# Kernel tuning notes

Hardware: AMD Instinct MI355X
Metric: run time of the kernel (lower is better)

Reference implementation:

```python
import jax, jax.numpy as jnp
import numpy as np

WS = 10      # window_size
HID = 32     # hidden_dim
B, T = 1024, 4096


def setup_inputs() -> dict:
    key = jax.random.key(0)
    k = jax.random.split(key, 7)
    returns = jax.random.normal(k[0], (B, T), dtype=jnp.float32) * 0.01
    W1 = jax.random.normal(k[1], (WS, HID), dtype=jnp.float32) * (1.0 / np.sqrt(WS))
    b1 = jnp.zeros((HID,), dtype=jnp.float32)
    W2 = jax.random.normal(k[2], (HID, HID), dtype=jnp.float32) * (1.0 / np.sqrt(HID))
    b2 = jnp.zeros((HID,), dtype=jnp.float32)
    W3 = jax.random.normal(k[3], (HID, 1), dtype=jnp.float32) * (1.0 / np.sqrt(HID))
    b3 = jnp.zeros((1,), dtype=jnp.float32)
    return {"returns": returns, "W1": W1, "b1": b1, "W2": W2, "b2": b2, "W3": W3, "b3": b3}


def reference(returns, W1, b1, W2, b2, W3, b3):
    ws = W1.shape[0]
    Bb, Tt = returns.shape
    # Unfold all sliding windows at once: windows[b, i, :] = returns[b, i:i+ws]
    # (window ending just before timestep t = i + ws)
    idx = jnp.arange(Tt - ws)[:, None] + jnp.arange(ws)[None, :]  # [T-ws, ws]
    windows = returns[:, idx]                                     # [B, T-ws, ws]
    h = jax.nn.relu(windows @ W1 + b1)                            # [B, T-ws, HID]
    h = jax.nn.relu(h @ W2 + b2)                                  # [B, T-ws, HID]
    out = 0.5 * jax.nn.sigmoid((h @ W3 + b3).squeeze(-1))         # [B, T-ws]
    # H_local[:, t] = out[:, t-ws] for t >= ws; first ws columns copy column ws
    head = jnp.broadcast_to(out[:, :1], (Bb, ws))                 # [B, ws]
    return jnp.concatenate([head, out], axis=1)                   # [B, T]
```

## Files before the change

kernel.cpp:

```cpp
#include <hip/hip_runtime.h>
#include <math.h>

typedef _Float16 f16x8  __attribute__((ext_vector_type(8)));
typedef _Float16 h2v    __attribute__((ext_vector_type(2)));
typedef float    f32x16 __attribute__((ext_vector_type(16)));
typedef float    f32x4  __attribute__((ext_vector_type(4)));
typedef __fp16   h2a    __attribute__((ext_vector_type(2)));
typedef unsigned u32x4  __attribute__((ext_vector_type(4)));

#define WS    10
#define HID   32
#define BDIM  256
#define NWAVE 4
#define GN    32
#define T_LEN 4096
#define NGRP  (T_LEN / GN)

__device__ inline unsigned pack2u(float a, float b) {
    h2a t = __builtin_amdgcn_cvt_pkrtz(a, b);
    return __builtin_bit_cast(unsigned, t);
}
__device__ inline unsigned relu2(unsigned u) {
    h2v x = __builtin_bit_cast(h2v, u);
    h2v z = {(_Float16)0.0f, (_Float16)0.0f};
    return __builtin_bit_cast(unsigned, __builtin_elementwise_max(x, z));
}

__global__ __launch_bounds__(BDIM, 4)
void hurst_row5(const float* __restrict__ returns,
                const float* __restrict__ W1, const float* __restrict__ b1,
                const float* __restrict__ W2, const float* __restrict__ b2,
                const float* __restrict__ W3, const float* __restrict__ b3,
                float* __restrict__ out)
{
    const int tid  = threadIdx.x;
    const int wid  = tid >> 6;
    const int lane = tid & 63;
    const int n    = lane & 31;
    const int hi   = lane >> 5;

    f32x16 b1v, b2v, b3v;
    #pragma unroll
    for (int i = 0; i < 4; ++i) {
        const f32x4 v1 = ((const f32x4*)b1)[2 * i + hi];
        const f32x4 v2 = ((const f32x4*)b2)[2 * i + hi];
        #pragma unroll
        for (int o = 0; o < 4; ++o) {
            b1v[4 * i + o] = v1[o];
            b2v[4 * i + o] = v2[o];
        }
    }
    const float b3s = b3[0];
    #pragma unroll
    for (int r = 0; r < 16; ++r) b3v[r] = b3s;

    f16x8 a1, a2lo, a2hi, a3lo, a3hi;
    #pragma unroll
    for (int jj = 0; jj < 8; ++jj) {
        const int k  = 8 * hi + jj;
        a1[jj] = (k < WS) ? (_Float16)W1[k * HID + n] : (_Float16)0.0f;
        const int kf = (k & 3) | ((k & 4) << 1) | ((k & 8) >> 1);
        a2lo[jj] = (_Float16)W2[kf * HID + n];
        a2hi[jj] = (_Float16)W2[(16 + kf) * HID + n];
        a3lo[jj] = (_Float16)W3[kf];
        a3hi[jj] = (_Float16)W3[16 + kf];
    }

    const float* rptr = returns + (size_t)blockIdx.x * T_LEN;
    float*       optr = out     + (size_t)blockIdx.x * T_LEN;

    const int t0  = wid * GN + n;
    int ws_c = (t0 >= WS) ? (t0 - WS) : 0;
    float e2_c[2], v6_c[6];
    __builtin_memcpy(e2_c, &rptr[ws_c + 8 * hi], 8);
    __builtin_memcpy(v6_c, &rptr[ws_c + 2], 24);

    for (int g = wid; g < NGRP; g += NWAVE) {
        const int gn_ = (g + NWAVE < NGRP) ? (g + NWAVE) : g;
        const int tn  = gn_ * GN + n;
        const int wsn = (tn >= WS) ? (tn - WS) : 0;
        float e2_n[2], v6_n[6];
        __builtin_memcpy(e2_n, &rptr[wsn + 8 * hi], 8);
        __builtin_memcpy(v6_n, &rptr[wsn + 2], 24);

        u32x4 xu;
        xu[0] = pack2u(e2_c[0], e2_c[1]);
        xu[1] = hi ? 0u : pack2u(v6_c[0], v6_c[1]);
        xu[2] = hi ? 0u : pack2u(v6_c[2], v6_c[3]);
        xu[3] = hi ? 0u : pack2u(v6_c[4], v6_c[5]);
        const f16x8 xb = __builtin_bit_cast(f16x8, xu);

        f32x16 d1 = __builtin_amdgcn_mfma_f32_32x32x16_f16(a1, xb, b1v, 0, 0, 0);

        u32x4 p1lo, p1hi;
        #pragma unroll
        for (int i = 0; i < 4; ++i) {
            p1lo[i] = relu2(pack2u(d1[2 * i],     d1[2 * i + 1]));
            p1hi[i] = relu2(pack2u(d1[8 + 2 * i], d1[9 + 2 * i]));
        }

        f32x16 d2 = __builtin_amdgcn_mfma_f32_32x32x16_f16(
                        a2lo, __builtin_bit_cast(f16x8, p1lo), b2v, 0, 0, 0);
        d2 = __builtin_amdgcn_mfma_f32_32x32x16_f16(
                        a2hi, __builtin_bit_cast(f16x8, p1hi), d2, 0, 0, 0);

        u32x4 p2lo, p2hi;
        #pragma unroll
        for (int i = 0; i < 4; ++i) {
            p2lo[i] = relu2(pack2u(d2[2 * i],     d2[2 * i + 1]));
            p2hi[i] = relu2(pack2u(d2[8 + 2 * i], d2[9 + 2 * i]));
        }

        f32x16 d3 = __builtin_amdgcn_mfma_f32_32x32x16_f16(
                        a3lo, __builtin_bit_cast(f16x8, p2lo), b3v, 0, 0, 0);
        d3 = __builtin_amdgcn_mfma_f32_32x32x16_f16(
                        a3hi, __builtin_bit_cast(f16x8, p2hi), d3, 0, 0, 0);

        const float o = 0.5f * __builtin_amdgcn_rcpf(1.0f + __expf(-d3[0]));
        if (hi == 0)
            optr[g * GN + n] = o;

        #pragma unroll
        for (int i = 0; i < 2; ++i) e2_c[i] = e2_n[i];
        #pragma unroll
        for (int i = 0; i < 6; ++i) v6_c[i] = v6_n[i];
    }
}

extern "C" void kernel_launch(void* const* d_in, const int* in_sizes, int n_in,
                              void* d_out, int out_size, void* d_ws, size_t ws_size,
                              hipStream_t stream) {
    const float* returns = (const float*)d_in[0];
    const float* W1      = (const float*)d_in[1];
    const float* b1      = (const float*)d_in[2];
    const float* W2      = (const float*)d_in[3];
    const float* b2      = (const float*)d_in[4];
    const float* W3      = (const float*)d_in[5];
    const float* b3      = (const float*)d_in[6];
    float* out = (float*)d_out;

    const int B = out_size / T_LEN;

    dim3 grid(B, 1, 1);
    dim3 block(BDIM, 1, 1);
    hurst_row5<<<grid, block, 0, stream>>>(returns, W1, b1, W2, b2, W3, b3, out);
}
```

Measured before the change: 101.8 us.

## Switch to grid-stride work distribution over all groups with persistent grid

Replaces the one-block-per-row mapping with a fixed grid of 1280 blocks whose waves stride over all 32-timestep groups across every row. Occupancy hint rises to 5 blocks per CU, the software prefetch of the next window is dropped, and the window loads are restructured into two 16-byte loads. The b3 bias vector register is removed by reusing b2v as the d3 accumulator and subtracting a scalar correction. The batch size of 1024 is hardcoded, so the kernel ignores out_size, and the prefetch removal exposes load latency.

```diff
diff --git a/kernel.cpp b/kernel.cpp
--- a/kernel.cpp
+++ b/kernel.cpp
@@ -8,13 +8,16 @@
 typedef __fp16   h2a    __attribute__((ext_vector_type(2)));
 typedef unsigned u32x4  __attribute__((ext_vector_type(4)));
 
-#define WS    10
-#define HID   32
-#define BDIM  256
-#define NWAVE 4
-#define GN    32
-#define T_LEN 4096
-#define NGRP  (T_LEN / GN)
+#define WS     10
+#define HID    32
+#define BDIM   256
+#define NWAVE  4
+#define GN     32
+#define T_LEN  4096
+#define GPR    (T_LEN / GN)
+#define NGTOT  (GPR * 1024)
+#define GRID   1280
+#define WSTRIDE (GRID * NWAVE)
 
 __device__ inline unsigned pack2u(float a, float b) {
     h2a t = __builtin_amdgcn_cvt_pkrtz(a, b);
@@ -26,12 +29,12 @@
     return __builtin_bit_cast(unsigned, __builtin_elementwise_max(x, z));
 }
 
-__global__ __launch_bounds__(BDIM, 4)
-void hurst_row5(const float* __restrict__ returns,
-                const float* __restrict__ W1, const float* __restrict__ b1,
-                const float* __restrict__ W2, const float* __restrict__ b2,
-                const float* __restrict__ W3, const float* __restrict__ b3,
-                float* __restrict__ out)
+__global__ __launch_bounds__(BDIM, 5)
+void hurst_wave5(const float* __restrict__ returns,
+                 const float* __restrict__ W1, const float* __restrict__ b1,
+                 const float* __restrict__ W2, const float* __restrict__ b2,
+                 const float* __restrict__ W3, const float* __restrict__ b3,
+                 float* __restrict__ out)
 {
     const int tid  = threadIdx.x;
     const int wid  = tid >> 6;
@@ -39,7 +42,7 @@
     const int n    = lane & 31;
     const int hi   = lane >> 5;
 
-    f32x16 b1v, b2v, b3v;
+    f32x16 b1v, b2v;
     #pragma unroll
     for (int i = 0; i < 4; ++i) {
         const f32x4 v1 = ((const f32x4*)b1)[2 * i + hi];
@@ -50,9 +53,7 @@
             b2v[4 * i + o] = v2[o];
         }
     }
-    const float b3s = b3[0];
-    #pragma unroll
-    for (int r = 0; r < 16; ++r) b3v[r] = b3s;
+    const float corr = b3[0] - b2[4 * hi];
 
     f16x8 a1, a2lo, a2hi, a3lo, a3hi;
     #pragma unroll
@@ -66,37 +67,32 @@
         a3hi[jj] = (_Float16)W3[16 + kf];
     }
 
-    const float* rptr = returns + (size_t)blockIdx.x * T_LEN;
-    float*       optr = out     + (size_t)blockIdx.x * T_LEN;
+    const int g0 = blockIdx.x * NWAVE + wid;
 
-    const int t0  = wid * GN + n;
-    int ws_c = (t0 >= WS) ? (t0 - WS) : 0;
-    float e2_c[2], v6_c[6];
-    __builtin_memcpy(e2_c, &rptr[ws_c + 8 * hi], 8);
-    __builtin_memcpy(v6_c, &rptr[ws_c + 2], 24);
+    for (int g = g0; g < NGTOT; g += WSTRIDE) {
+        const int   row  = g >> 7;
+        const int   tg   = (g & 127) * GN + n;
+        const int   ws   = (tg >= WS) ? (tg - WS) : 0;
+        const float* rp  = returns + (size_t)row * T_LEN;
 
-    for (int g = wid; g < NGRP; g += NWAVE) {
-        const int gn_ = (g + NWAVE < NGRP) ? (g + NWAVE) : g;
-        const int tn  = gn_ * GN + n;
-        const int wsn = (tn >= WS) ? (tn - WS) : 0;
-        float e2_n[2], v6_n[6];
-        __builtin_memcpy(e2_n, &rptr[wsn + 8 * hi], 8);
-        __builtin_memcpy(v6_n, &rptr[wsn + 2], 24);
+        float A[4], Bv[4];
+        __builtin_memcpy(A,  rp + ws + 6 * hi, 16);
+        __builtin_memcpy(Bv, rp + ws + 4,      16);
 
         u32x4 xu;
-        xu[0] = pack2u(e2_c[0], e2_c[1]);
-        xu[1] = hi ? 0u : pack2u(v6_c[0], v6_c[1]);
-        xu[2] = hi ? 0u : pack2u(v6_c[2], v6_c[3]);
-        xu[3] = hi ? 0u : pack2u(v6_c[4], v6_c[5]);
+        xu[0] = hi ? pack2u(A[2], A[3]) : pack2u(A[0], A[1]);
+        xu[1] = hi ? 0u : pack2u(A[2], A[3]);
+        xu[2] = hi ? 0u : pack2u(Bv[0], Bv[1]);
+        xu[3] = hi ? 0u : pack2u(Bv[2], Bv[3]);
         const f16x8 xb = __builtin_bit_cast(f16x8, xu);
 
         f32x16 d1 = __builtin_amdgcn_mfma_f32_32x32x16_f16(a1, xb, b1v, 0, 0, 0);
 
         u32x4 p1lo, p1hi;
         #pragma unroll
-        for (int i = 0; i < 4; ++i) {
-            p1lo[i] = relu2(pack2u(d1[2 * i],     d1[2 * i + 1]));
-            p1hi[i] = relu2(pack2u(d1[8 + 2 * i], d1[9 + 2 * i]));
+        for (int q = 0; q < 4; ++q) {
+            p1lo[q] = relu2(pack2u(d1[2 * q],     d1[2 * q + 1]));
+            p1hi[q] = relu2(pack2u(d1[8 + 2 * q], d1[9 + 2 * q]));
         }
 
         f32x16 d2 = __builtin_amdgcn_mfma_f32_32x32x16_f16(
@@ -106,24 +102,19 @@
 
         u32x4 p2lo, p2hi;
         #pragma unroll
-        for (int i = 0; i < 4; ++i) {
-            p2lo[i] = relu2(pack2u(d2[2 * i],     d2[2 * i + 1]));
-            p2hi[i] = relu2(pack2u(d2[8 + 2 * i], d2[9 + 2 * i]));
+        for (int q = 0; q < 4; ++q) {
+            p2lo[q] = relu2(pack2u(d2[2 * q],     d2[2 * q + 1]));
+            p2hi[q] = relu2(pack2u(d2[8 + 2 * q], d2[9 + 2 * q]));
         }
 
         f32x16 d3 = __builtin_amdgcn_mfma_f32_32x32x16_f16(
-                        a3lo, __builtin_bit_cast(f16x8, p2lo), b3v, 0, 0, 0);
+                        a3lo, __builtin_bit_cast(f16x8, p2lo), b2v, 0, 0, 0);
         d3 = __builtin_amdgcn_mfma_f32_32x32x16_f16(
                         a3hi, __builtin_bit_cast(f16x8, p2hi), d3, 0, 0, 0);
 
-        const float o = 0.5f * __builtin_amdgcn_rcpf(1.0f + __expf(-d3[0]));
+        const float o = 0.5f * __builtin_amdgcn_rcpf(1.0f + __expf(-(d3[0] + corr)));
         if (hi == 0)
-            optr[g * GN + n] = o;
-
-        #pragma unroll
-        for (int i = 0; i < 2; ++i) e2_c[i] = e2_n[i];
-        #pragma unroll
-        for (int i = 0; i < 6; ++i) v6_c[i] = v6_n[i];
+            out[(size_t)row * T_LEN + tg] = o;
     }
 }
 
@@ -139,9 +130,7 @@
     const float* b3      = (const float*)d_in[6];
     float* out = (float*)d_out;
 
-    const int B = out_size / T_LEN;
-
-    dim3 grid(B, 1, 1);
+    dim3 grid(GRID, 1, 1);
     dim3 block(BDIM, 1, 1);
-    hurst_row5<<<grid, block, 0, stream>>>(returns, W1, b1, W2, b2, W3, b3, out);
+    hurst_wave5<<<grid, block, 0, stream>>>(returns, W1, b1, W2, b2, W3, b3, out);
 }
```

Result: slower. 104.7 us (+2.9%).

## Stage fp16 row in LDS with shifted copy; reuse b2 as layer-3 accumulator

Applied to the files above, without the earlier changes.

Each block now loads its whole input row once with coalesced 64-byte per-thread loads. It converts the row to packed fp16 and stores it in LDS twice: once aligned and once shifted by one element, so every window can be read with a single aligned 16-byte LDS read. This replaces the per-iteration overlapping unaligned global loads and the register prefetch. The b3 broadcast register vector is dropped: the b2 bias vector is reused as the layer-3 accumulator seed and corrected by a scalar before the sigmoid. The change adds 16 KB of LDS per block and a __syncthreads, which may limit occupancy under launch_bounds(256,4).

```diff
diff --git a/kernel.cpp b/kernel.cpp
--- a/kernel.cpp
+++ b/kernel.cpp
@@ -15,6 +15,7 @@
 #define GN    32
 #define T_LEN 4096
 #define NGRP  (T_LEN / GN)
+#define PADN  4104
 
 __device__ inline unsigned pack2u(float a, float b) {
     h2a t = __builtin_amdgcn_cvt_pkrtz(a, b);
@@ -27,19 +28,21 @@
 }
 
 __global__ __launch_bounds__(BDIM, 4)
-void hurst_row5(const float* __restrict__ returns,
-                const float* __restrict__ W1, const float* __restrict__ b1,
-                const float* __restrict__ W2, const float* __restrict__ b2,
-                const float* __restrict__ W3, const float* __restrict__ b3,
-                float* __restrict__ out)
+void hurst_ldsrow(const float* __restrict__ returns,
+                  const float* __restrict__ W1, const float* __restrict__ b1,
+                  const float* __restrict__ W2, const float* __restrict__ b2,
+                  const float* __restrict__ W3, const float* __restrict__ b3,
+                  float* __restrict__ out)
 {
+    __shared__ __align__(16) _Float16 sbuf[2 * PADN];
+
     const int tid  = threadIdx.x;
     const int wid  = tid >> 6;
     const int lane = tid & 63;
     const int n    = lane & 31;
     const int hi   = lane >> 5;
 
-    f32x16 b1v, b2v, b3v;
+    f32x16 b1v, b2v;
     #pragma unroll
     for (int i = 0; i < 4; ++i) {
         const f32x4 v1 = ((const f32x4*)b1)[2 * i + hi];
@@ -50,9 +53,7 @@
             b2v[4 * i + o] = v2[o];
         }
     }
-    const float b3s = b3[0];
-    #pragma unroll
-    for (int r = 0; r < 16; ++r) b3v[r] = b3s;
+    const float corr = b3[0] - b2[4 * hi];
 
     f16x8 a1, a2lo, a2hi, a3lo, a3hi;
     #pragma unroll
@@ -66,37 +67,52 @@
         a3hi[jj] = (_Float16)W3[16 + kf];
     }
 
-    const float* rptr = returns + (size_t)blockIdx.x * T_LEN;
+    const float* rp   = returns + (size_t)blockIdx.x * T_LEN;
     float*       optr = out     + (size_t)blockIdx.x * T_LEN;
 
-    const int t0  = wid * GN + n;
-    int ws_c = (t0 >= WS) ? (t0 - WS) : 0;
-    float e2_c[2], v6_c[6];
-    __builtin_memcpy(e2_c, &rptr[ws_c + 8 * hi], 8);
-    __builtin_memcpy(v6_c, &rptr[ws_c + 2], 24);
+    {
+        float f[17];
+        __builtin_memcpy(f, rp + 16 * tid, 64);
+        const int nx = 16 * tid + 16;
+        f[16] = rp[(nx < T_LEN) ? nx : (T_LEN - 1)];
+
+        u32x4 q0a, q0b, q1a, q1b;
+        #pragma unroll
+        for (int k = 0; k < 4; ++k) {
+            q0a[k] = pack2u(f[2 * k],     f[2 * k + 1]);
+            q0b[k] = pack2u(f[8 + 2 * k], f[9 + 2 * k]);
+            q1a[k] = pack2u(f[2 * k + 1], f[2 * k + 2]);
+            q1b[k] = pack2u(f[9 + 2 * k], f[10 + 2 * k]);
+        }
+        unsigned* s32 = (unsigned*)sbuf;
+        *(u32x4*)(s32 + 8 * tid)                  = q0a;
+        *(u32x4*)(s32 + 8 * tid + 4)              = q0b;
+        *(u32x4*)(s32 + (PADN / 2) + 8 * tid)     = q1a;
+        *(u32x4*)(s32 + (PADN / 2) + 8 * tid + 4) = q1b;
+    }
+    __syncthreads();
 
     for (int g = wid; g < NGRP; g += NWAVE) {
-        const int gn_ = (g + NWAVE < NGRP) ? (g + NWAVE) : g;
-        const int tn  = gn_ * GN + n;
-        const int wsn = (tn >= WS) ? (tn - WS) : 0;
-        float e2_n[2], v6_n[6];
-        __builtin_memcpy(e2_n, &rptr[wsn + 8 * hi], 8);
-        __builtin_memcpy(v6_n, &rptr[wsn + 2], 24);
+        const int tg = g * GN + n;
+        const int ws = (tg >= WS) ? (tg - WS) : 0;
 
+        const unsigned eoff = (ws & 1) ? (unsigned)(PADN + ws - 1) : (unsigned)ws;
+        u32x4 q;
+        __builtin_memcpy(&q, (const char*)sbuf + 2 * eoff + 8 * hi, 16);
         u32x4 xu;
-        xu[0] = pack2u(e2_c[0], e2_c[1]);
-        xu[1] = hi ? 0u : pack2u(v6_c[0], v6_c[1]);
-        xu[2] = hi ? 0u : pack2u(v6_c[2], v6_c[3]);
-        xu[3] = hi ? 0u : pack2u(v6_c[4], v6_c[5]);
+        xu[0] = hi ? q[2] : q[0];
+        xu[1] = hi ? 0u   : q[1];
+        xu[2] = hi ? 0u   : q[2];
+        xu[3] = hi ? 0u   : q[3];
         const f16x8 xb = __builtin_bit_cast(f16x8, xu);
 
         f32x16 d1 = __builtin_amdgcn_mfma_f32_32x32x16_f16(a1, xb, b1v, 0, 0, 0);
 
         u32x4 p1lo, p1hi;
         #pragma unroll
-        for (int i = 0; i < 4; ++i) {
-            p1lo[i] = relu2(pack2u(d1[2 * i],     d1[2 * i + 1]));
-            p1hi[i] = relu2(pack2u(d1[8 + 2 * i], d1[9 + 2 * i]));
+        for (int qq = 0; qq < 4; ++qq) {
+            p1lo[qq] = relu2(pack2u(d1[2 * qq],     d1[2 * qq + 1]));
+            p1hi[qq] = relu2(pack2u(d1[8 + 2 * qq], d1[9 + 2 * qq]));
         }
 
         f32x16 d2 = __builtin_amdgcn_mfma_f32_32x32x16_f16(
@@ -106,24 +122,19 @@
 
         u32x4 p2lo, p2hi;
         #pragma unroll
-        for (int i = 0; i < 4; ++i) {
-            p2lo[i] = relu2(pack2u(d2[2 * i],     d2[2 * i + 1]));
-            p2hi[i] = relu2(pack2u(d2[8 + 2 * i], d2[9 + 2 * i]));
+        for (int qq = 0; qq < 4; ++qq) {
+            p2lo[qq] = relu2(pack2u(d2[2 * qq],     d2[2 * qq + 1]));
+            p2hi[qq] = relu2(pack2u(d2[8 + 2 * qq], d2[9 + 2 * qq]));
         }
 
         f32x16 d3 = __builtin_amdgcn_mfma_f32_32x32x16_f16(
-                        a3lo, __builtin_bit_cast(f16x8, p2lo), b3v, 0, 0, 0);
+                        a3lo, __builtin_bit_cast(f16x8, p2lo), b2v, 0, 0, 0);
         d3 = __builtin_amdgcn_mfma_f32_32x32x16_f16(
                         a3hi, __builtin_bit_cast(f16x8, p2hi), d3, 0, 0, 0);
 
-        const float o = 0.5f * __builtin_amdgcn_rcpf(1.0f + __expf(-d3[0]));
+        const float o = 0.5f * __builtin_amdgcn_rcpf(1.0f + __expf(-(d3[0] + corr)));
         if (hi == 0)
-            optr[g * GN + n] = o;
-
-        #pragma unroll
-        for (int i = 0; i < 2; ++i) e2_c[i] = e2_n[i];
-        #pragma unroll
-        for (int i = 0; i < 6; ++i) v6_c[i] = v6_n[i];
+            optr[tg] = o;
     }
 }
 
@@ -143,5 +154,5 @@
 
     dim3 grid(B, 1, 1);
     dim3 block(BDIM, 1, 1);
-    hurst_row5<<<grid, block, 0, stream>>>(returns, W1, b1, W2, b2, W3, b3, out);
+    hurst_ldsrow<<<grid, block, 0, stream>>>(returns, W1, b1, W2, b2, W3, b3, out);
 }
```

After: 99.55 us. 2.2% less time.
